# Performance work log

Measured on AMD Instinct MI355X. Metric: run time of the kernel, lower is better.

Reference implementation:

```python
import jax, jax.numpy as jnp
import numpy as np
from jax import lax

N, M, D = 16384, 4096, 256
CHUNK = 64  # chunk over N for the elementwise min to avoid the O(N*M*D) intermediate


def setup_inputs() -> dict:
    key = jax.random.key(0)
    kz, ke = jax.random.split(key)
    z = jax.random.normal(kz, (N, D), dtype=jnp.float32)
    e = jax.random.normal(ke, (M, D), dtype=jnp.float32)
    return {"z": z, "e": e}


def reference(z, e):
    # --- min_loss: mean over codebook entries of min over latents of squared L2 distance ---
    # GEMM trick: ||z-e||^2 = ||z||^2 + ||e||^2 - 2 z.e
    z2 = jnp.sum(z * z, axis=1)           # [N]
    e2 = jnp.sum(e * e, axis=1)           # [M]
    d2 = z2[:, None] + e2[None, :] - 2.0 * (z @ e.T)  # [N, M]
    min_loss = jnp.mean(jnp.min(d2, axis=0))

    # --- wise_min_loss: mean over (M, D) of elementwise min over N of (z_i - e_j)^2 ---
    # scan over chunks of N with a running min to avoid materializing [N, M, D]
    zc = z.reshape(N // CHUNK, CHUNK, D)
    def step(carry, zb):
        d = (zb[:, None, :] - e[None, :, :]) ** 2  # [CHUNK, M, D]
        return jnp.minimum(carry, jnp.min(d, axis=0)), None
    init = jnp.full((M, D), jnp.inf, dtype=z.dtype)
    wise_min, _ = lax.scan(step, init, zc)  # [M, D]
    wise_min_loss = jnp.mean(wise_min)

    return min_loss, wise_min_loss
```

## Files before the change

### kernel.cpp

```cpp
#include <hip/hip_runtime.h>
#include <hip/hip_bf16.h>

#define N_Z 16384
#define M_E 4096
#define DIM 256
#define NB5 1024
#define BMIN (-6.0f)
#define SCALE5 ((float)NB5 / 12.0f)

typedef __bf16 bf16x8 __attribute__((ext_vector_type(8)));
typedef float f32x4 __attribute__((ext_vector_type(4)));

__device__ __forceinline__ unsigned short f2bf(float f) {
  unsigned u = __float_as_uint(f);
  u = (u + 0x7FFFu + ((u >> 16) & 1u)) >> 16;
  return (unsigned short)u;
}

__device__ __forceinline__ void gl2lds16(const void* g, void* s) {
  __builtin_amdgcn_global_load_lds(
      (const __attribute__((address_space(1))) unsigned*)g,
      (__attribute__((address_space(3))) unsigned*)s, 16, 0, 0);
}

__device__ __forceinline__ unsigned fmap(float f) {
  unsigned u = __float_as_uint(f);
  return (u & 0x80000000u) ? ~u : (u | 0x80000000u);
}
__device__ __forceinline__ float funmap(unsigned u) {
  return __uint_as_float((u & 0x80000000u) ? (u ^ 0x80000000u) : ~u);
}
__device__ __forceinline__ int bucket5(float v) {
  int b = (int)((v - BMIN) * SCALE5);
  return min(max(b, 0), NB5 - 1);
}

__global__ void init_kernel(unsigned* __restrict__ d2min, float* __restrict__ wise_part) {
  int i = blockIdx.x * blockDim.x + threadIdx.x;
  if (i < M_E) d2min[i] = 0x7F800000u;
  if (i < 64) wise_part[i] = 0.0f;
}

__global__ __launch_bounds__(256) void prep2_kernel(
    const float* __restrict__ z, const float* __restrict__ e,
    float* __restrict__ zT, float* __restrict__ eT,
    unsigned short* __restrict__ zb, unsigned short* __restrict__ eb,
    float* __restrict__ z2, float* __restrict__ e2) {
  __shared__ float tile[32][33];
  int rblk = blockIdx.x * 32;
  const float* in;
  float* outT;
  unsigned short* outB;
  float* rsum;
  int R, r0;
  if (rblk < N_Z) {
    in = z; outT = zT; outB = zb; rsum = z2; R = N_Z; r0 = rblk;
  } else {
    in = e; outT = eT; outB = eb; rsum = e2; R = M_E; r0 = rblk - N_Z;
  }
  int tx = threadIdx.x, ty = threadIdx.y;
  float acc[4] = {0.f, 0.f, 0.f, 0.f};
#pragma unroll 1
  for (int cc = 0; cc < DIM; cc += 32) {
#pragma unroll
    for (int i = 0; i < 4; ++i) {
      int rr = ty + 8 * i;
      float v = in[(size_t)(r0 + rr) * DIM + cc + tx];
      tile[rr][tx] = v;
      outB[(size_t)(r0 + rr) * DIM + cc + tx] = f2bf(v);
      acc[i] += v * v;
    }
    __syncthreads();
#pragma unroll
    for (int i = 0; i < 4; ++i)
      outT[(size_t)(cc + ty + 8 * i) * R + r0 + tx] = tile[tx][ty + 8 * i];
    __syncthreads();
  }
#pragma unroll
  for (int i = 0; i < 4; ++i) {
    float s = acc[i];
#pragma unroll
    for (int o = 1; o < 32; o <<= 1) s += __shfl_xor(s, o);
    if (tx == 0) rsum[r0 + ty + 8 * i] = s;
  }
}

__global__ __launch_bounds__(256, 2) void gemm_min_kernel(
    const unsigned short* __restrict__ zb, const unsigned short* __restrict__ eb,
    const float* __restrict__ z2, const float* __restrict__ e2,
    unsigned* __restrict__ d2min) {
  __shared__ __align__(16) unsigned short lA[128 * 64];
  __shared__ __align__(16) unsigned short lB[128 * 64];

  const int t = threadIdx.x;
  const int w = t >> 6;
  const int l = t & 63;
  const int wr = w >> 1, wc = w & 1;
  int flat = blockIdx.y * 32 + blockIdx.x;
  int nf = (flat >> 3) + (flat & 7) * 512;
  const int tileM = (nf & 31) * 128;
  const int tileN = (nf >> 5) * 128;
  const int l15 = l & 15;
  const int kgr = l >> 4;

  f32x4 acc[4][4];
#pragma unroll
  for (int i = 0; i < 4; ++i)
#pragma unroll
    for (int j = 0; j < 4; ++j) acc[i][j] = (f32x4){0.f, 0.f, 0.f, 0.f};

#pragma unroll 1
  for (int k0 = 0; k0 < DIM; k0 += 64) {
#pragma unroll
    for (int i = 0; i < 4; ++i) {
      int c = i * 256 + t;
      int row = c >> 3;
      int kc = c & 7;
      int kcs = kc ^ (row & 7);
      int ldsbase = (i * 256 + (t & ~63)) * 8;
      gl2lds16(zb + (size_t)(tileN + row) * DIM + (k0 + kcs * 8), &lA[ldsbase]);
      gl2lds16(eb + (size_t)(tileM + row) * DIM + (k0 + kcs * 8), &lB[ldsbase]);
    }
    __syncthreads();

#pragma unroll
    for (int kk = 0; kk < 2; ++kk) {
      bf16x8 a[4], b[4];
      const int kcr = kk * 4 + kgr;
#pragma unroll
      for (int mi = 0; mi < 4; ++mi) {
        int row = wr * 64 + mi * 16 + l15;
        a[mi] = *(const bf16x8*)&lA[row * 64 + ((kcr ^ (row & 7)) * 8)];
      }
#pragma unroll
      for (int ni = 0; ni < 4; ++ni) {
        int row = wc * 64 + ni * 16 + l15;
        b[ni] = *(const bf16x8*)&lB[row * 64 + ((kcr ^ (row & 7)) * 8)];
      }
#pragma unroll
      for (int mi = 0; mi < 4; ++mi)
#pragma unroll
        for (int ni = 0; ni < 4; ++ni)
          acc[mi][ni] = __builtin_amdgcn_mfma_f32_16x16x32_bf16(a[mi], b[ni], acc[mi][ni], 0, 0, 0);
    }
    __syncthreads();
  }

  float* z2s = (float*)lA;
  if (t < 128) z2s[t] = z2[tileN + t];
  __syncthreads();

#pragma unroll
  for (int ni = 0; ni < 4; ++ni) {
    float v = 3.4e38f;
#pragma unroll
    for (int mi = 0; mi < 4; ++mi)
#pragma unroll
      for (int r = 0; r < 4; ++r) {
        int rloc = wr * 64 + mi * 16 + kgr * 4 + r;
        v = fminf(v, z2s[rloc] - 2.0f * acc[mi][ni][r]);
      }
    v = fminf(v, __shfl_xor(v, 16));
    v = fminf(v, __shfl_xor(v, 32));
    if (l < 16) {
      int m = tileM + wc * 64 + ni * 16 + l;
      float d2 = v + e2[m];
      atomicMin(&d2min[m], __float_as_uint(d2));
    }
  }
}

__global__ __launch_bounds__(1024) void wise8_kernel(
    const float* __restrict__ zT, const float* __restrict__ eT,
    float* __restrict__ wise_part) {
  extern __shared__ __align__(16) char smem[];
  float* zs = (float*)smem;
  unsigned* zoff = (unsigned*)(smem + 65536);
  unsigned* pmax = zoff + NB5;
  unsigned* psminN = pmax + NB5;
  float* esorted = zs;
  unsigned* eoff = zoff;
  __shared__ unsigned scr[16];

  const int d = blockIdx.x, t = threadIdx.x;
  const int lane = t & 63, wid = t >> 6;

  eoff[t] = 0u;
  __syncthreads();
  const float* ec = eT + (size_t)d * M_E;
  float ev4[4];
  int ebk[4];
#pragma unroll
  for (int i = 0; i < 4; ++i) {
    ev4[i] = ec[i * 1024 + t];
    ebk[i] = bucket5(ev4[i]);
    atomicAdd(&eoff[ebk[i]], 1u);
  }
  __syncthreads();
  {
    unsigned c = eoff[t];
    unsigned incl = c;
#pragma unroll
    for (int o = 1; o < 64; o <<= 1) {
      unsigned v = __shfl_up(incl, o);
      if (lane >= o) incl += v;
    }
    if (lane == 63) scr[wid] = incl;
    __syncthreads();
    if (t == 0) {
      unsigned run = 0;
#pragma unroll
      for (int i = 0; i < 16; ++i) { unsigned v = scr[i]; scr[i] = run; run += v; }
    }
    __syncthreads();
    unsigned excl = scr[wid] + incl - c;
    __syncthreads();
    eoff[t] = excl;
  }
  __syncthreads();
#pragma unroll
  for (int i = 0; i < 4; ++i) {
    unsigned pos = atomicAdd(&eoff[ebk[i]], 1u);
    esorted[pos] = ev4[i];
  }
  __syncthreads();
  float eq[4];
#pragma unroll
  for (int q = 0; q < 4; ++q) eq[q] = esorted[q * 1024 + t];
  __syncthreads();

  zoff[t] = 0u;
  __syncthreads();

  float zv[16];
  int zbk[16];
  const float4* p = (const float4*)(zT + (size_t)d * N_Z);
#pragma unroll
  for (int i = 0; i < 4; ++i) {
    float4 v = p[i * 1024 + t];
    zv[4 * i + 0] = v.x; zv[4 * i + 1] = v.y; zv[4 * i + 2] = v.z; zv[4 * i + 3] = v.w;
  }
#pragma unroll
  for (int i = 0; i < 16; ++i) {
    zbk[i] = bucket5(zv[i]);
    atomicAdd(&zoff[zbk[i]], 1u);
  }
  __syncthreads();

  {
    unsigned c = zoff[t];
    unsigned incl = c;
#pragma unroll
    for (int o = 1; o < 64; o <<= 1) {
      unsigned v = __shfl_up(incl, o);
      if (lane >= o) incl += v;
    }
    if (lane == 63) scr[wid] = incl;
    __syncthreads();
    if (t == 0) {
      unsigned run = 0;
#pragma unroll
      for (int i = 0; i < 16; ++i) { unsigned v = scr[i]; scr[i] = run; run += v; }
    }
    __syncthreads();
    unsigned excl = scr[wid] + incl - c;
    __syncthreads();
    zoff[t] = excl;
  }
  __syncthreads();

#pragma unroll
  for (int i = 0; i < 16; ++i) {
    unsigned pos = atomicAdd(&zoff[zbk[i]], 1u);
    zs[pos] = zv[i];
  }
  __syncthreads();

  {
    unsigned s0 = t ? zoff[t - 1] : 0u;
    unsigned s1 = zoff[t];
    unsigned mxU = 0u, mnN = 0u;
    for (unsigned j = s0; j < s1; ++j) {
      unsigned u = fmap(zs[j]);
      mxU = max(mxU, u);
      mnN = max(mnN, ~u);
    }
    pmax[t] = mxU;
    psminN[t] = mnN;
  }
  __syncthreads();

  {
    unsigned s = pmax[t];
    unsigned incl = s;
#pragma unroll
    for (int o = 1; o < 64; o <<= 1) {
      unsigned v = __shfl_up(incl, o);
      if (lane >= o) incl = max(incl, v);
    }
    __syncthreads();
    if (lane == 63) scr[wid] = incl;
    __syncthreads();
    if (t == 0) {
      unsigned run = 0;
#pragma unroll
      for (int i = 0; i < 16; ++i) { unsigned v = scr[i]; scr[i] = run; run = max(run, v); }
    }
    __syncthreads();
    pmax[t] = max(scr[wid], incl);
  }
  {
    int tr = NB5 - 1 - t;
    unsigned s = psminN[tr];
    unsigned incl = s;
#pragma unroll
    for (int o = 1; o < 64; o <<= 1) {
      unsigned v = __shfl_up(incl, o);
      if (lane >= o) incl = max(incl, v);
    }
    __syncthreads();
    if (lane == 63) scr[wid] = incl;
    __syncthreads();
    if (t == 0) {
      unsigned run = 0;
#pragma unroll
      for (int i = 0; i < 16; ++i) { unsigned v = scr[i]; scr[i] = run; run = max(run, v); }
    }
    __syncthreads();
    psminN[tr] = max(scr[wid], incl);
  }
  __syncthreads();

  float accq = 0.0f;
#pragma unroll 1
  for (int q = 0; q < 4; ++q) {
    float ev = eq[q];
    int b0 = bucket5(ev);
    unsigned s0 = b0 ? zoff[b0 - 1] : 0u;
    unsigned s1 = zoff[b0];
    float best2 = 3.4e38f;
    if (b0 > 0) {
      unsigned u = pmax[b0 - 1];
      if (u) { float dd = funmap(u) - ev; best2 = dd * dd; }
    }
    if (b0 < NB5 - 1) {
      unsigned u = psminN[b0 + 1];
      if (u) { float dd = funmap(~u) - ev; best2 = fminf(best2, dd * dd); }
    }
    for (unsigned j = s0 & ~3u; j < s1; j += 4) {
      float4 zz = *(const float4*)&zs[j];
      float d0 = zz.x - ev, d1 = zz.y - ev;
      float d2 = zz.z - ev, d3 = zz.w - ev;
      best2 = fminf(best2, fminf(fminf(d0 * d0, d1 * d1), fminf(d2 * d2, d3 * d3)));
    }
    accq += best2;
  }

#pragma unroll
  for (int o = 32; o; o >>= 1) accq += __shfl_down(accq, o);
  __syncthreads();
  if (lane == 0) scr[wid] = __float_as_uint(accq);
  __syncthreads();
  if (t == 0) {
    float ssum = 0.0f;
#pragma unroll
    for (int i = 0; i < 16; ++i) ssum += __uint_as_float(scr[i]);
    atomicAdd(&wise_part[d & 63], ssum);
  }
}

__global__ void final_kernel(const unsigned* __restrict__ d2min,
                             const float* __restrict__ wise_part, float* __restrict__ out) {
  __shared__ float red[4];
  int t = threadIdx.x;
  float s = 0.0f;
  for (int m = t; m < M_E; m += 256) s += __uint_as_float(d2min[m]);
#pragma unroll
  for (int off = 32; off; off >>= 1) s += __shfl_down(s, off);
  if ((t & 63) == 0) red[t >> 6] = s;
  __syncthreads();
  if (t == 0) {
    float tot = red[0] + red[1] + red[2] + red[3];
    out[0] = tot / (float)M_E;
    float w = 0.0f;
    for (int i = 0; i < 64; ++i) w += wise_part[i];
    out[1] = w / ((float)M_E * (float)DIM);
  }
}

extern "C" void kernel_launch(void* const* d_in, const int* in_sizes, int n_in,
                              void* d_out, int out_size, void* d_ws, size_t ws_size,
                              hipStream_t stream) {
  const float* z = (const float*)d_in[0];
  const float* e = (const float*)d_in[1];
  float* out = (float*)d_out;

  char* ws = (char*)d_ws;
  unsigned short* zb = (unsigned short*)ws;
  unsigned short* eb = (unsigned short*)(ws + 8388608);
  float* z2 = (float*)(ws + 10485760);
  float* e2 = (float*)(ws + 10551296);
  unsigned* d2min = (unsigned*)(ws + 10567680);
  float* wise_part = (float*)(ws + 10584064);
  float* zT = (float*)(ws + 11534336);
  float* eT = (float*)(ws + 28311552);

  const size_t LDS_WISE = 65536 + 3 * NB5 * 4;
  static int attr_done = 0;
  if (!attr_done) {
    (void)hipFuncSetAttribute((const void*)wise8_kernel,
                              hipFuncAttributeMaxDynamicSharedMemorySize, (int)LDS_WISE);
    attr_done = 1;
  }

  init_kernel<<<16, 256, 0, stream>>>(d2min, wise_part);
  prep2_kernel<<<(N_Z + M_E) / 32, dim3(32, 8), 0, stream>>>(z, e, zT, eT, zb, eb, z2, e2);
  gemm_min_kernel<<<dim3(32, 128), 256, 0, stream>>>(zb, eb, z2, e2, d2min);
  wise8_kernel<<<DIM, 1024, LDS_WISE, stream>>>(zT, eT, wise_part);
  final_kernel<<<1, 256, 0, stream>>>(d2min, wise_part, out);
}
```

Baseline: 137.5 us.

## Fold init and final reduction into neighbors, enlarge GEMM tile to 256x256

Moves the d2min/wise_part initialization into the first block of the prep kernel and the final reduction into the last-finishing wise8 block via an atomic completion counter, removing two kernel launches. Separately, the GEMM-min kernel now uses 256x256 tiles with 512 threads (8 waves, each holding 8x4 MFMA accumulators), halving the number of atomicMin writes and increasing operand reuse. The larger tile raises register and LDS pressure and cuts occupancy, and the grid shrinks to 1024 blocks.

```diff
diff --git a/kernel.cpp b/kernel.cpp
--- a/kernel.cpp
+++ b/kernel.cpp
@@ -35,19 +35,22 @@
   return min(max(b, 0), NB5 - 1);
 }
 
-__global__ void init_kernel(unsigned* __restrict__ d2min, float* __restrict__ wise_part) {
-  int i = blockIdx.x * blockDim.x + threadIdx.x;
-  if (i < M_E) d2min[i] = 0x7F800000u;
-  if (i < 64) wise_part[i] = 0.0f;
-}
-
 __global__ __launch_bounds__(256) void prep2_kernel(
     const float* __restrict__ z, const float* __restrict__ e,
     float* __restrict__ zT, float* __restrict__ eT,
     unsigned short* __restrict__ zb, unsigned short* __restrict__ eb,
-    float* __restrict__ z2, float* __restrict__ e2) {
+    float* __restrict__ z2, float* __restrict__ e2,
+    unsigned* __restrict__ d2min, float* __restrict__ wise_part,
+    unsigned* __restrict__ wfin) {
   __shared__ float tile[32][33];
   int rblk = blockIdx.x * 32;
+  int tx = threadIdx.x, ty = threadIdx.y;
+  int lt = ty * 32 + tx;
+  if (blockIdx.x == 0) {
+    for (int i = lt; i < M_E; i += 256) d2min[i] = 0x7F800000u;
+    if (lt < 64) wise_part[lt] = 0.0f;
+    if (lt == 0) *wfin = 0u;
+  }
   const float* in;
   float* outT;
   unsigned short* outB;
@@ -58,7 +61,6 @@
   } else {
     in = e; outT = eT; outB = eb; rsum = e2; R = M_E; r0 = rblk - N_Z;
   }
-  int tx = threadIdx.x, ty = threadIdx.y;
   float acc[4] = {0.f, 0.f, 0.f, 0.f};
 #pragma unroll 1
   for (int cc = 0; cc < DIM; cc += 32) {
@@ -85,27 +87,28 @@
   }
 }
 
-__global__ __launch_bounds__(256, 2) void gemm_min_kernel(
+__global__ __launch_bounds__(512) void gemm_min2_kernel(
     const unsigned short* __restrict__ zb, const unsigned short* __restrict__ eb,
     const float* __restrict__ z2, const float* __restrict__ e2,
     unsigned* __restrict__ d2min) {
-  __shared__ __align__(16) unsigned short lA[128 * 64];
-  __shared__ __align__(16) unsigned short lB[128 * 64];
+  __shared__ __align__(16) unsigned short lA[256 * 64];
+  __shared__ __align__(16) unsigned short lB[256 * 64];
 
   const int t = threadIdx.x;
   const int w = t >> 6;
   const int l = t & 63;
-  const int wr = w >> 1, wc = w & 1;
-  int flat = blockIdx.y * 32 + blockIdx.x;
-  int nf = (flat >> 3) + (flat & 7) * 512;
-  const int tileM = (nf & 31) * 128;
-  const int tileN = (nf >> 5) * 128;
+  const int wr = w >> 2;
+  const int wc = w & 3;
+  int flat = blockIdx.y * 16 + blockIdx.x;
+  int nf = (flat >> 3) + (flat & 7) * 128;
+  const int tileM = (nf & 15) * 256;
+  const int tileN = (nf >> 4) * 256;
   const int l15 = l & 15;
   const int kgr = l >> 4;
 
-  f32x4 acc[4][4];
-#pragma unroll
-  for (int i = 0; i < 4; ++i)
+  f32x4 acc[8][4];
+#pragma unroll
+  for (int i = 0; i < 8; ++i)
 #pragma unroll
     for (int j = 0; j < 4; ++j) acc[i][j] = (f32x4){0.f, 0.f, 0.f, 0.f};
 
@@ -113,11 +116,11 @@
   for (int k0 = 0; k0 < DIM; k0 += 64) {
 #pragma unroll
     for (int i = 0; i < 4; ++i) {
-      int c = i * 256 + t;
+      int c = i * 512 + t;
       int row = c >> 3;
       int kc = c & 7;
       int kcs = kc ^ (row & 7);
-      int ldsbase = (i * 256 + (t & ~63)) * 8;
+      int ldsbase = (i * 512 + (t & ~63)) * 8;
       gl2lds16(zb + (size_t)(tileN + row) * DIM + (k0 + kcs * 8), &lA[ldsbase]);
       gl2lds16(eb + (size_t)(tileM + row) * DIM + (k0 + kcs * 8), &lB[ldsbase]);
     }
@@ -125,11 +128,11 @@
 
 #pragma unroll
     for (int kk = 0; kk < 2; ++kk) {
-      bf16x8 a[4], b[4];
+      bf16x8 a[8], b[4];
       const int kcr = kk * 4 + kgr;
 #pragma unroll
-      for (int mi = 0; mi < 4; ++mi) {
-        int row = wr * 64 + mi * 16 + l15;
+      for (int mi = 0; mi < 8; ++mi) {
+        int row = wr * 128 + mi * 16 + l15;
         a[mi] = *(const bf16x8*)&lA[row * 64 + ((kcr ^ (row & 7)) * 8)];
       }
 #pragma unroll
@@ -138,7 +141,7 @@
         b[ni] = *(const bf16x8*)&lB[row * 64 + ((kcr ^ (row & 7)) * 8)];
       }
 #pragma unroll
-      for (int mi = 0; mi < 4; ++mi)
+      for (int mi = 0; mi < 8; ++mi)
 #pragma unroll
         for (int ni = 0; ni < 4; ++ni)
           acc[mi][ni] = __builtin_amdgcn_mfma_f32_16x16x32_bf16(a[mi], b[ni], acc[mi][ni], 0, 0, 0);
@@ -147,17 +150,17 @@
   }
 
   float* z2s = (float*)lA;
-  if (t < 128) z2s[t] = z2[tileN + t];
+  if (t < 256) z2s[t] = z2[tileN + t];
   __syncthreads();
 
 #pragma unroll
   for (int ni = 0; ni < 4; ++ni) {
     float v = 3.4e38f;
 #pragma unroll
-    for (int mi = 0; mi < 4; ++mi)
+    for (int mi = 0; mi < 8; ++mi)
 #pragma unroll
       for (int r = 0; r < 4; ++r) {
-        int rloc = wr * 64 + mi * 16 + kgr * 4 + r;
+        int rloc = wr * 128 + mi * 16 + kgr * 4 + r;
         v = fminf(v, z2s[rloc] - 2.0f * acc[mi][ni][r]);
       }
     v = fminf(v, __shfl_xor(v, 16));
@@ -172,7 +175,8 @@
 
 __global__ __launch_bounds__(1024) void wise8_kernel(
     const float* __restrict__ zT, const float* __restrict__ eT,
-    float* __restrict__ wise_part) {
+    float* __restrict__ wise_part, const unsigned* __restrict__ d2min,
+    unsigned* __restrict__ wfin, float* __restrict__ out) {
   extern __shared__ __align__(16) char smem[];
   float* zs = (float*)smem;
   unsigned* zoff = (unsigned*)(smem + 65536);
@@ -361,30 +365,35 @@
   __syncthreads();
   if (lane == 0) scr[wid] = __float_as_uint(accq);
   __syncthreads();
+
+  __shared__ unsigned amLast;
   if (t == 0) {
     float ssum = 0.0f;
 #pragma unroll
     for (int i = 0; i < 16; ++i) ssum += __uint_as_float(scr[i]);
     atomicAdd(&wise_part[d & 63], ssum);
-  }
-}
-
-__global__ void final_kernel(const unsigned* __restrict__ d2min,
-                             const float* __restrict__ wise_part, float* __restrict__ out) {
-  __shared__ float red[4];
-  int t = threadIdx.x;
-  float s = 0.0f;
-  for (int m = t; m < M_E; m += 256) s += __uint_as_float(d2min[m]);
-#pragma unroll
-  for (int off = 32; off; off >>= 1) s += __shfl_down(s, off);
-  if ((t & 63) == 0) red[t >> 6] = s;
-  __syncthreads();
-  if (t == 0) {
-    float tot = red[0] + red[1] + red[2] + red[3];
-    out[0] = tot / (float)M_E;
-    float w = 0.0f;
-    for (int i = 0; i < 64; ++i) w += wise_part[i];
-    out[1] = w / ((float)M_E * (float)DIM);
+    __threadfence();
+    amLast = (atomicAdd(wfin, 1u) == (unsigned)(DIM - 1)) ? 1u : 0u;
+  }
+  __syncthreads();
+  if (amLast) {
+    __threadfence();
+    float s = 0.0f;
+    for (int m = t; m < M_E; m += 1024) s += __uint_as_float(d2min[m]);
+#pragma unroll
+    for (int o = 32; o; o >>= 1) s += __shfl_down(s, o);
+    __syncthreads();
+    if (lane == 0) scr[wid] = __float_as_uint(s);
+    __syncthreads();
+    if (t == 0) {
+      float tot = 0.0f;
+#pragma unroll
+      for (int i = 0; i < 16; ++i) tot += __uint_as_float(scr[i]);
+      out[0] = tot / (float)M_E;
+      float wsum = 0.0f;
+      for (int i = 0; i < 64; ++i) wsum += wise_part[i];
+      out[1] = wsum / ((float)M_E * (float)DIM);
+    }
   }
 }
 
@@ -402,6 +411,7 @@
   float* e2 = (float*)(ws + 10551296);
   unsigned* d2min = (unsigned*)(ws + 10567680);
   float* wise_part = (float*)(ws + 10584064);
+  unsigned* wfin = (unsigned*)(ws + 10584320);
   float* zT = (float*)(ws + 11534336);
   float* eT = (float*)(ws + 28311552);
 
@@ -413,9 +423,8 @@
     attr_done = 1;
   }
 
-  init_kernel<<<16, 256, 0, stream>>>(d2min, wise_part);
-  prep2_kernel<<<(N_Z + M_E) / 32, dim3(32, 8), 0, stream>>>(z, e, zT, eT, zb, eb, z2, e2);
-  gemm_min_kernel<<<dim3(32, 128), 256, 0, stream>>>(zb, eb, z2, e2, d2min);
-  wise8_kernel<<<DIM, 1024, LDS_WISE, stream>>>(zT, eT, wise_part);
-  final_kernel<<<1, 256, 0, stream>>>(d2min, wise_part, out);
-}
+  prep2_kernel<<<(N_Z + M_E) / 32, dim3(32, 8), 0, stream>>>(z, e, zT, eT, zb, eb, z2, e2,
+                                                             d2min, wise_part, wfin);
+  gemm_min2_kernel<<<dim3(16, 64), 512, 0, stream>>>(zb, eb, z2, e2, d2min);
+  wise8_kernel<<<DIM, 1024, LDS_WISE, stream>>>(zT, eT, wise_part, d2min, wfin, out);
+}
```

After: 146.7 us. 6.7% more time.
